# Optimization experiments

Measured on AMD Instinct MI355X. Metric: run time of the kernel, lower is better.

Reference implementation:

```python
import jax, jax.numpy as jnp
import numpy as np

EMBED_DIM = 768
NUM_HEADS = 12
PROJ_DIM = EMBED_DIM // NUM_HEADS  # 64
M_FEATURES = 128
EPS = 1e-6


def _orthogonal_projection(key, m, d):
    # Faithful to create_projection_matrix(scaling=0): stacked transposed Q-factors
    # of iid gaussian blocks, rescaled by chi-distributed row norms.
    nb_full_blocks = m // d
    keys = jax.random.split(key, nb_full_blocks + 2)
    blocks = []
    for i in range(nb_full_blocks):
        q, _ = jnp.linalg.qr(jax.random.normal(keys[i], (d, d)))
        blocks.append(q.T)
    rem = m - nb_full_blocks * d
    if rem > 0:
        q, _ = jnp.linalg.qr(jax.random.normal(keys[nb_full_blocks], (d, d)))
        blocks.append(q.T[:rem])
    final = jnp.vstack(blocks)
    multiplier = jnp.linalg.norm(jax.random.normal(keys[-1], (m, d)), axis=1)
    return multiplier[:, None] * final


def setup_inputs() -> dict:
    key = jax.random.key(0)
    ks = jax.random.split(key, 8)
    B, L, E = 4, 4096, EMBED_DIM
    s = 1.0 / np.sqrt(E)
    inp = {
        "x": jax.random.normal(ks[0], (B, L, E), jnp.float32),
        "Wq": jax.random.normal(ks[1], (E, E), jnp.float32) * s,
        "bq": jnp.zeros((E,), jnp.float32),
        "Wk": jax.random.normal(ks[2], (E, E), jnp.float32) * s,
        "bk": jnp.zeros((E,), jnp.float32),
        "Wv": jax.random.normal(ks[3], (E, E), jnp.float32) * s,
        "bv": jnp.zeros((E,), jnp.float32),
        "Wo": jax.random.normal(ks[4], (E, E), jnp.float32) * s,
        "bo": jnp.zeros((E,), jnp.float32),
        "proj": _orthogonal_projection(ks[5], M_FEATURES, PROJ_DIM),
    }
    return inp


def _softmax_kernel(data, projection_matrix):
    # data: [B, L, H, D]; projection_matrix: [M, D]
    data_normalizer = 1.0 / jnp.sqrt(jnp.sqrt(jnp.float32(PROJ_DIM)))
    data = data_normalizer * data
    ratio = 1.0 / jnp.sqrt(jnp.float32(projection_matrix.shape[0]))
    data_dash = jnp.einsum("blhd,md->blhm", data, projection_matrix)
    diag_data = jnp.sum(jnp.square(data), axis=-1, keepdims=True) / 2.0  # [B,L,H,1]
    stab = jnp.max(data_dash, axis=-1, keepdims=True)
    return ratio * (jnp.exp(data_dash - diag_data - stab) + EPS)


def reference(x, Wq, bq, Wk, bk, Wv, bv, Wo, bo, proj):
    B, L, E = x.shape
    H, D = NUM_HEADS, PROJ_DIM

    def split_heads(t):
        return t.reshape(B, L, H, D)

    q = split_heads(x @ Wq + bq)
    k = split_heads(x @ Wk + bk)
    v = split_heads(x @ Wv + bv)

    q_prime = _softmax_kernel(q, proj)  # [B,L,H,M]
    k_prime = _softmax_kernel(k, proj)  # [B,L,H,M]

    # Linear-attention numerator/denominator (O(L) in sequence length).
    kvs = jnp.einsum("blhm,blhd->bhmd", k_prime, v)          # [B,H,M,D]
    num = jnp.einsum("blhm,bhmd->blhd", q_prime, kvs)        # [B,L,H,D]
    ks_sum = jnp.sum(k_prime, axis=1)                         # [B,H,M]
    den = jnp.einsum("blhm,bhm->blh", q_prime, ks_sum)        # [B,L,H]
    attention = num / den[..., None]                          # [B,L,H,D]

    # Faithful to source: transpose to [B,H,L,D] then reshape to [B,-1,E].
    concat = jnp.transpose(attention, (0, 2, 1, 3)).reshape(B, -1, E)
    return concat @ Wo + bo
```

## Files before the change

### kernel.cpp

```cpp
#include <hip/hip_runtime.h>

typedef _Float16 f16;
typedef __attribute__((ext_vector_type(8))) _Float16 half8;
typedef __attribute__((ext_vector_type(4))) _Float16 half4;
typedef __attribute__((ext_vector_type(4))) float f32x4;

#define DEVINL static __device__ __forceinline__

constexpr float NORMALIZER = 0.35355339059327373f;
constexpr float RATIO      = 0.08838834764831845f;
constexpr float FEPS       = 1e-6f;

constexpr size_t OFF_WQKVT = 0;
constexpr size_t OFF_WOT   = OFF_WQKVT + (size_t)2304*768*2;
constexpr size_t OFF_PROJF = OFF_WOT   + (size_t)768*768*2;
constexpr size_t OFF_KS    = OFF_PROJF + (size_t)128*64*2;
constexpr size_t OFF_KSP   = OFF_KS    + (size_t)48*128*4;
constexpr size_t OFF_DEN   = OFF_KSP   + (size_t)48*64*128*4;
constexpr size_t OFF_KVST  = OFF_DEN   + (size_t)48*4096*4;
constexpr size_t OFF_KVSP  = OFF_KVST  + (size_t)48*64*128*2;
constexpr size_t OFF_X16   = OFF_KVSP  + (size_t)8*48*128*64*4;
constexpr size_t OFF_ATT   = OFF_X16;
constexpr size_t OFF_Q16   = OFF_X16 + (size_t)16384*768*2;
constexpr size_t OFF_K16   = OFF_Q16 + (size_t)16384*768*2;
constexpr size_t OFF_VT    = OFF_K16 + (size_t)16384*768*2;
constexpr size_t OFF_QP    = OFF_K16;
constexpr size_t OFF_KPT   = OFF_VT  + (size_t)16384*768*2;

DEVINL void gload_lds16(const f16* g, f16* lds) {
  __builtin_amdgcn_global_load_lds(
      (const __attribute__((address_space(1))) void*)g,
      (__attribute__((address_space(3))) void*)lds, 16, 0, 0);
}

#define VMCNT(n)  asm volatile("s_waitcnt vmcnt(" #n ")" ::: "memory")
#define LGKMCNT0  asm volatile("s_waitcnt lgkmcnt(0)" ::: "memory")
#define SCHEDB    __builtin_amdgcn_sched_barrier(0)
#define BAR       __builtin_amdgcn_s_barrier()

DEVINL void gemm8p_core(const f16* __restrict__ Ag, const f16* __restrict__ Bg,
                        f16* smem, f32x4 (&acc)[8][4], int w, int lane)
{
  constexpr int NT = 12;
  const int wm = w >> 2, wn = w & 3;
  const int c = lane & 15, g16 = lane >> 4;

#pragma unroll
  for (int i = 0; i < 8; ++i)
#pragma unroll
    for (int j = 0; j < 4; ++j)
      acc[i][j] = f32x4{0.f, 0.f, 0.f, 0.f};

  auto STG = [&](const f16* g, int koff, f16* ldsbase) {
#pragma unroll
    for (int u = 0; u < 2; ++u) {
      const int r = w * 32 + u * 16 + (lane >> 2);
      const int sg = lane & 3;
      gload_lds16(g + (size_t)r * 768 + koff + ((sg ^ ((r ^ (r >> 2)) & 3)) << 3),
                  ldsbase + (w * 128 + u * 64) * 8);
    }
  };
  auto RDA = [&](const f16* kbase, int mh, half8 (&av)[4]) {
#pragma unroll
    for (int i = 0; i < 4; ++i) {
      const int r = wm * 128 + mh * 64 + i * 16 + c;
      av[i] = *(const half8*)(kbase + r * 32 + ((g16 ^ ((r ^ (r >> 2)) & 3)) << 3));
    }
  };
  auto RDB = [&](const f16* kbase, half8 (&bv)[4]) {
#pragma unroll
    for (int j = 0; j < 4; ++j) {
      const int col = wn * 64 + j * 16 + c;
      bv[j] = *(const half8*)(kbase + 16384 + col * 32 + ((g16 ^ ((col ^ (col >> 2)) & 3)) << 3));
    }
  };
  auto MF0 = [&](const half8 (&av)[4], const half8 (&bv)[4]) {
    __builtin_amdgcn_s_setprio(1);
#pragma unroll
    for (int i = 0; i < 4; ++i)
#pragma unroll
      for (int j = 0; j < 4; ++j)
        acc[i][j] = __builtin_amdgcn_mfma_f32_16x16x32_f16(av[i], bv[j], acc[i][j], 0, 0, 0);
    __builtin_amdgcn_s_setprio(0);
  };
  auto MF1 = [&](const half8 (&av)[4], const half8 (&bv)[4]) {
    __builtin_amdgcn_s_setprio(1);
#pragma unroll
    for (int i = 0; i < 4; ++i)
#pragma unroll
      for (int j = 0; j < 4; ++j)
        acc[4 + i][j] = __builtin_amdgcn_mfma_f32_16x16x32_f16(av[i], bv[j], acc[4 + i][j], 0, 0, 0);
    __builtin_amdgcn_s_setprio(0);
  };

  STG(Ag, 0, smem);
  STG(Bg, 0, smem + 16384);
  STG(Ag, 32, smem + 8192);
  STG(Bg, 32, smem + 16384 + 8192);
  VMCNT(0);
  BAR; SCHEDB;

#pragma unroll 1
  for (int t = 0; t < NT; ++t) {
    f16* bufR = smem + (t & 1) * 32768;
    f16* bufW = smem + ((t & 1) ^ 1) * 32768;
    const int kn = (t + 1) * 64;
    const bool st = (t + 1) < NT;
    half8 av[4], bv[4];

    RDA(bufR, 0, av); RDB(bufR, bv);
    if (st) STG(Ag, kn, bufW);
    SCHEDB; BAR; LGKMCNT0; SCHEDB;
    MF0(av, bv);
    BAR; SCHEDB;
    RDA(bufR, 1, av);
    if (st) STG(Bg, kn, bufW + 16384);
    SCHEDB; BAR; LGKMCNT0; SCHEDB;
    MF1(av, bv);
    if (st) { VMCNT(4); } else { VMCNT(0); }
    BAR; SCHEDB;
    RDA(bufR + 8192, 0, av); RDB(bufR + 8192, bv);
    if (st) STG(Ag, kn + 32, bufW + 8192);
    SCHEDB; BAR; LGKMCNT0; SCHEDB;
    MF0(av, bv);
    BAR; SCHEDB;
    RDA(bufR + 8192, 1, av);
    if (st) STG(Bg, kn + 32, bufW + 16384 + 8192);
    SCHEDB; BAR; LGKMCNT0; SCHEDB;
    MF1(av, bv);
    if (st) { VMCNT(4); }
    BAR; SCHEDB;
  }
}

__global__ __launch_bounds__(512, 2) void k_gemm_qkv4(const f16* __restrict__ X16, const f16* __restrict__ WT,
    const float* __restrict__ bq, const float* __restrict__ bk, const float* __restrict__ bv,
    f16* __restrict__ Qo, f16* __restrict__ Ko, f16* __restrict__ VT)
{
  __shared__ f16 smem[65536];
  f32x4 acc[8][4];
  const int lin = blockIdx.x;
  const int xcd = lin & 7, idx = lin >> 3;
  const int bx = xcd * 8 + idx / 9;
  const int by = idx % 9;
  const int brow0 = bx * 256;
  const int t = threadIdx.x, w = t >> 6, lane = t & 63;
  gemm8p_core(X16 + (size_t)brow0 * 768, WT + (size_t)by * 256 * 768, smem, acc, w, lane);

  const int wm = w >> 2, wn = w & 3;
  const int c = lane & 15, g16 = lane >> 4;
  const int which = by / 3;
  const int colhdr = (by % 3) * 256;
  const float* bias = which == 0 ? bq : (which == 1 ? bk : bv);
  float bb[4];
#pragma unroll
  for (int j = 0; j < 4; ++j) bb[j] = bias[colhdr + wn * 64 + j * 16 + c];

  f16* ep = smem;
  if (which < 2) {
    f16* QK = which == 0 ? Qo : Ko;
#pragma unroll 1
    for (int p = 0; p < 2; ++p) {
      __syncthreads();
      if (wm == p) {
#pragma unroll
        for (int ii = 0; ii < 8; ++ii)
#pragma unroll
          for (int j = 0; j < 4; ++j)
#pragma unroll
            for (int r = 0; r < 4; ++r)
              ep[((ii >> 2) * 64 + (ii & 3) * 16 + g16 * 4 + r) * 264 + wn * 64 + j * 16 + c]
                  = (f16)(acc[ii][j][r] + bb[j]);
      }
      __syncthreads();
      const int row = threadIdx.x >> 2, seg = (threadIdx.x & 3) * 64;
      f16* dst = QK + (size_t)(brow0 + p * 128 + row) * 768 + colhdr + seg;
      const f16* sp = ep + row * 264 + seg;
#pragma unroll
      for (int u = 0; u < 4; ++u) *(half8*)(dst + u * 8) = *(const half8*)(sp + u * 8);
#pragma unroll
      for (int u = 4; u < 8; ++u) *(half8*)(dst + u * 8) = *(const half8*)(sp + u * 8);
    }
  } else {
    const int bIdx = brow0 >> 12;
#pragma unroll 1
    for (int ch = 0; ch < 2; ++ch) {
      __syncthreads();
      if ((wn >> 1) == ch) {
        const int cih0 = (wn & 1) * 64;
#pragma unroll
        for (int ii = 0; ii < 8; ++ii)
#pragma unroll
          for (int j = 0; j < 4; ++j)
#pragma unroll
            for (int r = 0; r < 4; ++r)
              ep[(cih0 + j * 16 + c) * 264 + wm * 128 + (ii >> 2) * 64 + (ii & 3) * 16 + g16 * 4 + r]
                  = (f16)(acc[ii][j][r] + bb[j]);
      }
      __syncthreads();
      const int cl = threadIdx.x >> 2, seg = (threadIdx.x & 3) * 64;
      const int vcol = colhdr + ch * 128 + cl;
      const int h = vcol >> 6, d = vcol & 63;
      f16* dst = VT + ((size_t)(bIdx * 12 + h) * 64 + d) * 4096 + (brow0 & 4095) + seg;
      const f16* sp = ep + cl * 264 + seg;
#pragma unroll
      for (int u = 0; u < 8; ++u) *(half8*)(dst + u * 8) = *(const half8*)(sp + u * 8);
    }
  }
}

__global__ __launch_bounds__(512, 2) void k_gemm_out4(const f16* __restrict__ ATT, const f16* __restrict__ WOT,
    const float* __restrict__ bo, float* __restrict__ out)
{
  __shared__ f16 smem[65536];
  f32x4 acc[8][4];
  const int lin = blockIdx.x;
  const int xcd = lin & 7, idx = lin >> 3;
  const int bx = xcd * 8 + idx / 3;
  const int by = idx % 3;
  const int brow0 = bx * 256;
  const int t = threadIdx.x, w = t >> 6, lane = t & 63;
  gemm8p_core(ATT + (size_t)brow0 * 768, WOT + (size_t)by * 256 * 768, smem, acc, w, lane);

  const int wm = w >> 2, wn = w & 3;
  const int c = lane & 15, g16 = lane >> 4;
  float bb[4];
#pragma unroll
  for (int j = 0; j < 4; ++j) bb[j] = bo[by * 256 + wn * 64 + j * 16 + c];
#pragma unroll
  for (int ii = 0; ii < 8; ++ii) {
    const int row0 = brow0 + wm * 128 + (ii >> 2) * 64 + (ii & 3) * 16 + g16 * 4;
#pragma unroll
    for (int j = 0; j < 4; ++j) {
      const int col = by * 256 + wn * 64 + j * 16 + c;
#pragma unroll
      for (int r = 0; r < 4; ++r)
        out[(size_t)(row0 + r) * 768 + col] = acc[ii][j][r] + bb[j];
    }
  }
}

template<int BN>
DEVINL void gemm_tile(const f16* A, int lda, const f16* Bt, int ldb, int K,
                      f16* As, f16* Bs, f32x4 (&acc)[4][BN/32])
{
  constexpr int NF = BN/32;
  const int t = threadIdx.x;
  const int w = t >> 6, lane = t & 63;
  const int g = lane >> 4, c = lane & 15;
  const int wr = w >> 1, wc = w & 1;
  const int srow = lane >> 2;
  const int sseg = (lane & 3) * 8;

#pragma unroll
  for (int i = 0; i < 4; ++i)
#pragma unroll
    for (int j = 0; j < NF; ++j)
      acc[i][j] = f32x4{0.f, 0.f, 0.f, 0.f};

  for (int k0 = 0; k0 < K; k0 += 32) {
#pragma unroll
    for (int r = 0; r < 2; ++r) {
      const int rowblk = (w + 4*r) * 16;
      gload_lds16(A + (size_t)(rowblk + srow) * lda + k0 + sseg, As + rowblk*32);
    }
#pragma unroll
    for (int r = 0; r < BN/64; ++r) {
      const int rowblk = (w + 4*r) * 16;
      gload_lds16(Bt + (size_t)(rowblk + srow) * ldb + k0 + sseg, Bs + rowblk*32);
    }
    __syncthreads();
    half8 av[4], bv[NF];
#pragma unroll
    for (int i = 0; i < 4; ++i)
      av[i] = *(const half8*)(As + (wr*64 + i*16 + c)*32 + g*8);
#pragma unroll
    for (int j = 0; j < NF; ++j)
      bv[j] = *(const half8*)(Bs + (wc*(BN/2) + j*16 + c)*32 + g*8);
#pragma unroll
    for (int i = 0; i < 4; ++i)
#pragma unroll
      for (int j = 0; j < NF; ++j)
        acc[i][j] = __builtin_amdgcn_mfma_f32_16x16x32_f16(av[i], bv[j], acc[i][j], 0, 0, 0);
    __syncthreads();
  }
}

__global__ __launch_bounds__(256) void k_cast_x(const float* __restrict__ X, f16* __restrict__ X16)
{
  const size_t i = ((size_t)blockIdx.x*256 + threadIdx.x) * 4;
  const float4 v = *(const float4*)(X + i);
  half4 h;
  h[0] = (f16)v.x; h[1] = (f16)v.y; h[2] = (f16)v.z; h[3] = (f16)v.w;
  *(half4*)(X16 + i) = h;
}

__global__ __launch_bounds__(256) void k_transpose_w(const float* __restrict__ W, f16* __restrict__ Wt)
{
  __shared__ float ls[64][65];
  const int t = threadIdx.x;
  const int k0 = blockIdx.x*64, n0 = blockIdx.y*64;
#pragma unroll
  for (int it = 0; it < 4; ++it) {
    const int r = it*16 + (t >> 4);
    const int cs = (t & 15) * 4;
    const float4 v = *(const float4*)(W + (size_t)(k0 + r)*768 + n0 + cs);
    ls[r][cs+0] = v.x; ls[r][cs+1] = v.y; ls[r][cs+2] = v.z; ls[r][cs+3] = v.w;
  }
  __syncthreads();
  const int n = t >> 2;
  const int seg = (t & 3) * 16;
  half8 ov[2];
#pragma unroll
  for (int i = 0; i < 16; ++i) ov[i>>3][i&7] = (f16)ls[seg + i][n];
  f16* dst = Wt + (size_t)(n0 + n)*768 + k0 + seg;
  *(half8*)dst = ov[0];
  *(half8*)(dst + 8) = ov[1];
}

__global__ __launch_bounds__(256) void k_cast_proj(const float* __restrict__ P, f16* __restrict__ PF)
{
  const int i = blockIdx.x*256 + threadIdx.x;
  PF[i] = (f16)(NORMALIZER * P[i]);
}

DEVINL void feat_common(const f16* base, const f16* PROJF,
                        f16* qs, f16* ps, float* dd, float* diag_s)
{
  const int t = threadIdx.x, w = t >> 6, lane = t & 63;
#pragma unroll
  for (int it = 0; it < 2; ++it) {
    const int rowblk = it*32 + w*8;
    gload_lds16(base + (size_t)(rowblk + (lane>>3))*768 + (lane&7)*8, qs + rowblk*64);
  }
#pragma unroll
  for (int it = 0; it < 4; ++it) {
    const int rowblk = it*32 + w*8;
    gload_lds16(PROJF + (size_t)(rowblk + (lane>>3))*64 + (lane&7)*8, ps + rowblk*64);
  }
  __syncthreads();
  if (t < 64) {
    float s = 0.f;
    for (int d = 0; d < 64; ++d) { const float qv = (float)qs[t*64 + d]; s += qv*qv; }
    diag_s[t] = 0.0625f * s;
  }
  const int g = lane >> 4, c = lane & 15;
  const int wr = w >> 1, wc = w & 1;
  f32x4 facc[2][4];
#pragma unroll
  for (int i = 0; i < 2; ++i)
#pragma unroll
    for (int j = 0; j < 4; ++j) facc[i][j] = f32x4{0.f,0.f,0.f,0.f};
#pragma unroll
  for (int kk = 0; kk < 2; ++kk) {
    half8 av[2], bv[4];
#pragma unroll
    for (int i = 0; i < 2; ++i) av[i] = *(const half8*)(qs + (wr*32 + i*16 + c)*64 + kk*32 + g*8);
#pragma unroll
    for (int j = 0; j < 4; ++j) bv[j] = *(const half8*)(ps + (wc*64 + j*16 + c)*64 + kk*32 + g*8);
#pragma unroll
    for (int i = 0; i < 2; ++i)
#pragma unroll
      for (int j = 0; j < 4; ++j)
        facc[i][j] = __builtin_amdgcn_mfma_f32_16x16x32_f16(av[i], bv[j], facc[i][j], 0, 0, 0);
  }
#pragma unroll
  for (int i = 0; i < 2; ++i)
#pragma unroll
    for (int j = 0; j < 4; ++j)
#pragma unroll
      for (int r = 0; r < 4; ++r)
        dd[(wr*32 + i*16 + g*4 + r)*129 + wc*64 + j*16 + c] = facc[i][j][r];
  __syncthreads();
}

__global__ __launch_bounds__(256) void k_qfeat(const f16* __restrict__ Q, const f16* __restrict__ PROJF,
    const float* __restrict__ KS, f16* __restrict__ QP, float* __restrict__ DEN)
{
  __shared__ f16 qs[64*64];
  __shared__ f16 ps[128*64];
  __shared__ float dd[64*129];
  __shared__ float diag_s[64];
  __shared__ float ks_s[128];
  const int t = threadIdx.x;
  const int lb = blockIdx.x, bh = blockIdx.y;
  const int b = bh / 12, h = bh - b*12;
  if (t < 128) ks_s[t] = KS[bh*128 + t];
  feat_common(Q + ((size_t)(b*4096 + lb*64))*768 + h*64, PROJF, qs, ps, dd, diag_s);
  const int l = t >> 2, s = t & 3;
  float v[32];
#pragma unroll
  for (int j = 0; j < 32; ++j) v[j] = dd[l*129 + s*32 + j];
  float mx = v[0];
#pragma unroll
  for (int j = 1; j < 32; ++j) mx = fmaxf(mx, v[j]);
  mx = fmaxf(mx, __shfl_xor(mx, 1));
  mx = fmaxf(mx, __shfl_xor(mx, 2));
  const float off = diag_s[l] + mx;
  half8 ov[4];
  float dp = 0.f;
#pragma unroll
  for (int j = 0; j < 32; ++j) {
    const float e = RATIO * (__expf(v[j] - off) + FEPS);
    ov[j>>3][j&7] = (f16)e;
    dp += e * ks_s[s*32 + j];
  }
  dp += __shfl_xor(dp, 1);
  dp += __shfl_xor(dp, 2);
  const size_t lrow = (size_t)bh*4096 + lb*64 + l;
  if (s == 0) DEN[lrow] = dp;
  f16* dst = QP + lrow*128 + s*32;
#pragma unroll
  for (int q8 = 0; q8 < 4; ++q8) *(half8*)(dst + q8*8) = ov[q8];
}

__global__ __launch_bounds__(256) void k_kfeat(const f16* __restrict__ Kin, const f16* __restrict__ PROJF,
    f16* __restrict__ KPT, float* __restrict__ KSP)
{
  __shared__ f16 qs[64*64];
  __shared__ f16 ps[128*64];
  __shared__ float dd[64*129];
  __shared__ float diag_s[64];
  const int t = threadIdx.x;
  const int lb = blockIdx.x, bh = blockIdx.y;
  const int b = bh / 12, h = bh - b*12;
  feat_common(Kin + ((size_t)(b*4096 + lb*64))*768 + h*64, PROJF, qs, ps, dd, diag_s);
  const int l = t >> 2, s = t & 3;
  float v[32];
#pragma unroll
  for (int j = 0; j < 32; ++j) v[j] = dd[l*129 + s*32 + j];
  float mx = v[0];
#pragma unroll
  for (int j = 1; j < 32; ++j) mx = fmaxf(mx, v[j]);
  mx = fmaxf(mx, __shfl_xor(mx, 1));
  mx = fmaxf(mx, __shfl_xor(mx, 2));
  const float off = diag_s[l] + mx;
#pragma unroll
  for (int j = 0; j < 32; ++j) dd[l*129 + s*32 + j] = RATIO * (__expf(v[j] - off) + FEPS);
  __syncthreads();
  if (t < 128) {
    float sm = 0.f;
    for (int l2 = 0; l2 < 64; ++l2) sm += dd[l2*129 + t];
    KSP[((size_t)bh*64 + lb)*128 + t] = sm;
  }
  const int m = t >> 1, hf = t & 1;
  half8 ov[4];
#pragma unroll
  for (int i2 = 0; i2 < 32; ++i2) ov[i2>>3][i2&7] = (f16)dd[(hf*32 + i2)*129 + m];
  f16* dst = KPT + ((size_t)bh*128 + m)*4096 + lb*64 + hf*32;
#pragma unroll
  for (int q8 = 0; q8 < 4; ++q8) *(half8*)(dst + q8*8) = ov[q8];
}

__global__ __launch_bounds__(256) void k_kvs(const f16* __restrict__ KPT, const f16* __restrict__ VT,
    float* __restrict__ KVSP)
{
  __shared__ f16 As[128*32], Bs[64*32];
  f32x4 acc[4][2];
  const int chunk = blockIdx.x, bh = blockIdx.y;
  gemm_tile<64>(KPT + (size_t)bh*128*4096 + chunk*512, 4096,
                VT  + (size_t)bh*64*4096  + chunk*512, 4096, 512, As, Bs, acc);
  const int t = threadIdx.x, w = t>>6, lane = t&63, g = lane>>4, c = lane&15;
  const int wr = w>>1, wc = w&1;
  float* dst = KVSP + (size_t)(chunk*48 + bh)*128*64;
#pragma unroll
  for (int i = 0; i < 4; ++i) {
    const int row0 = wr*64 + i*16 + g*4;
#pragma unroll
    for (int j = 0; j < 2; ++j) {
      const int col = wc*32 + j*16 + c;
#pragma unroll
      for (int r = 0; r < 4; ++r) dst[(size_t)(row0 + r)*64 + col] = acc[i][j][r];
    }
  }
}

__global__ __launch_bounds__(256) void k_reduce(const float* __restrict__ KVSP, const float* __restrict__ KSP,
    f16* __restrict__ KVST, float* __restrict__ KS)
{
  const int i = blockIdx.x*256 + threadIdx.x;
  if (i < 48*128*64) {
    const int bh = i >> 13, md = i & 8191, m = md >> 6, d = md & 63;
    float s = 0.f;
#pragma unroll
    for (int c = 0; c < 8; ++c) s += KVSP[((size_t)(c*48 + bh)*128 + m)*64 + d];
    KVST[((size_t)bh*64 + d)*128 + m] = (f16)s;
  }
  if (i < 48*128) {
    const int bh = i >> 7, m = i & 127;
    float s = 0.f;
#pragma unroll 8
    for (int lb = 0; lb < 64; ++lb) s += KSP[((size_t)bh*64 + lb)*128 + m];
    KS[i] = s;
  }
}

__global__ __launch_bounds__(256) void k_num(const f16* __restrict__ QP, const f16* __restrict__ KVST,
    const float* __restrict__ DEN, f16* __restrict__ ATT)
{
  __shared__ f16 As[128*32], Bs[64*32];
  f32x4 acc[4][2];
  const int bx = blockIdx.x, bh = blockIdx.y;
  gemm_tile<64>(QP + ((size_t)bh*4096 + bx*128)*128, 128,
                KVST + (size_t)bh*64*128, 128, 128, As, Bs, acc);
  const int t = threadIdx.x, w = t>>6, lane = t&63, g = lane>>4, c = lane&15;
  const int wr = w>>1, wc = w&1;
#pragma unroll
  for (int i = 0; i < 4; ++i) {
    const int l0 = bx*128 + wr*64 + i*16 + g*4;
#pragma unroll
    for (int j = 0; j < 2; ++j) {
      const int d = wc*32 + j*16 + c;
#pragma unroll
      for (int r = 0; r < 4; ++r) {
        const float den = DEN[(size_t)bh*4096 + l0 + r];
        ATT[((size_t)bh*4096 + l0 + r)*64 + d] = (f16)(acc[i][j][r] / den);
      }
    }
  }
}

extern "C" void kernel_launch(void* const* d_in, const int* in_sizes, int n_in,
                              void* d_out, int out_size, void* d_ws, size_t ws_size,
                              hipStream_t stream)
{
  const float* x    = (const float*)d_in[0];
  const float* Wq   = (const float*)d_in[1];
  const float* bq   = (const float*)d_in[2];
  const float* Wk   = (const float*)d_in[3];
  const float* bk   = (const float*)d_in[4];
  const float* Wv   = (const float*)d_in[5];
  const float* bv   = (const float*)d_in[6];
  const float* Wo   = (const float*)d_in[7];
  const float* bo   = (const float*)d_in[8];
  const float* proj = (const float*)d_in[9];
  float* out = (float*)d_out;
  char* ws = (char*)d_ws;

  f16*   WQKVT = (f16*)(ws + OFF_WQKVT);
  f16*   WOT   = (f16*)(ws + OFF_WOT);
  f16*   PROJF = (f16*)(ws + OFF_PROJF);
  float* KS    = (float*)(ws + OFF_KS);
  float* KSP   = (float*)(ws + OFF_KSP);
  float* DEN   = (float*)(ws + OFF_DEN);
  f16*   KVST  = (f16*)(ws + OFF_KVST);
  float* KVSP  = (float*)(ws + OFF_KVSP);
  f16*   X16   = (f16*)(ws + OFF_X16);
  f16*   ATT   = (f16*)(ws + OFF_ATT);
  f16*   Q16   = (f16*)(ws + OFF_Q16);
  f16*   K16   = (f16*)(ws + OFF_K16);
  f16*   VT    = (f16*)(ws + OFF_VT);
  f16*   QP    = (f16*)(ws + OFF_QP);
  f16*   KPT   = (f16*)(ws + OFF_KPT);

  k_cast_x<<<12288, 256, 0, stream>>>(x, X16);
  k_transpose_w<<<dim3(12,12), 256, 0, stream>>>(Wq, WQKVT);
  k_transpose_w<<<dim3(12,12), 256, 0, stream>>>(Wk, WQKVT + (size_t)768*768);
  k_transpose_w<<<dim3(12,12), 256, 0, stream>>>(Wv, WQKVT + (size_t)2*768*768);
  k_transpose_w<<<dim3(12,12), 256, 0, stream>>>(Wo, WOT);
  k_cast_proj<<<32, 256, 0, stream>>>(proj, PROJF);

  k_gemm_qkv4<<<576, 512, 0, stream>>>(X16, WQKVT, bq, bk, bv, Q16, K16, VT);
  k_kfeat<<<dim3(64,48), 256, 0, stream>>>(K16, PROJF, KPT, KSP);
  k_kvs<<<dim3(8,48), 256, 0, stream>>>(KPT, VT, KVSP);
  k_reduce<<<1536, 256, 0, stream>>>(KVSP, KSP, KVST, KS);
  k_qfeat<<<dim3(64,48), 256, 0, stream>>>(Q16, PROJF, KS, QP, DEN);
  k_num<<<dim3(32,48), 256, 0, stream>>>(QP, KVST, DEN, ATT);
  k_gemm_out4<<<192, 512, 0, stream>>>(ATT, WOT, bo, out);
}
```

Baseline: 283.5 us.

## Retile GEMMs to 256x192 blocks and fuse Q features with numerator

The shared GEMM core moves from 256x256 to 256x192 tiles, with a new swizzled LDS layout and smaller LDS. This raises the QKV grid to 768 blocks and the output GEMM grid to 256, so wave quantization across CUs improves. The Q feature map, denominator and numerator GEMM are fused into one kernel, k_qfn, which keeps QP and DEN in LDS instead of writing them to global memory and reading them back. The trade-offs are more LDS per feature block and less reuse per GEMM tile.

```diff
diff --git a/kernel.cpp b/kernel.cpp
--- a/kernel.cpp
+++ b/kernel.cpp
@@ -24,7 +24,6 @@
 constexpr size_t OFF_Q16   = OFF_X16 + (size_t)16384*768*2;
 constexpr size_t OFF_K16   = OFF_Q16 + (size_t)16384*768*2;
 constexpr size_t OFF_VT    = OFF_K16 + (size_t)16384*768*2;
-constexpr size_t OFF_QP    = OFF_K16;
 constexpr size_t OFF_KPT   = OFF_VT  + (size_t)16384*768*2;
 
 DEVINL void gload_lds16(const f16* g, f16* lds) {
@@ -38,123 +37,140 @@
 #define SCHEDB    __builtin_amdgcn_sched_barrier(0)
 #define BAR       __builtin_amdgcn_s_barrier()
 
-DEVINL void gemm8p_core(const f16* __restrict__ Ag, const f16* __restrict__ Bg,
-                        f16* smem, f32x4 (&acc)[8][4], int w, int lane)
+DEVINL void gemm192_core(const f16* __restrict__ Ag, const f16* __restrict__ Bg,
+                         f16* smem, f32x4 (&acc)[8][3], int w, int lane)
 {
   constexpr int NT = 12;
   const int wm = w >> 2, wn = w & 3;
   const int c = lane & 15, g16 = lane >> 4;
+  const int tid = threadIdx.x;
 
 #pragma unroll
   for (int i = 0; i < 8; ++i)
 #pragma unroll
-    for (int j = 0; j < 4; ++j)
+    for (int j = 0; j < 3; ++j)
       acc[i][j] = f32x4{0.f, 0.f, 0.f, 0.f};
 
-  auto STG = [&](const f16* g, int koff, f16* ldsbase) {
+  auto SA = [&](int tt, int kh, f16* buf) {
+    f16* dst = buf + kh * 8192;
 #pragma unroll
     for (int u = 0; u < 2; ++u) {
-      const int r = w * 32 + u * 16 + (lane >> 2);
-      const int sg = lane & 3;
-      gload_lds16(g + (size_t)r * 768 + koff + ((sg ^ ((r ^ (r >> 2)) & 3)) << 3),
-                  ldsbase + (w * 128 + u * 64) * 8);
+      const int id = u * 512 + tid;
+      const int r = id >> 2, sg = id & 3;
+      const int seg = sg ^ ((r >> 1) & 3);
+      gload_lds16(Ag + (size_t)r * 768 + tt * 64 + kh * 32 + seg * 8,
+                  dst + (u * 512 + w * 64) * 8);
     }
   };
-  auto RDA = [&](const f16* kbase, int mh, half8 (&av)[4]) {
+  auto SB = [&](int tt, f16* buf) {
+    f16* dst = buf + 16384;
+#pragma unroll
+    for (int u = 0; u < 3; ++u) {
+      const int id = u * 512 + tid;
+      const int r = id >> 3, sg = id & 7;
+      const int seg = sg ^ (r & 7);
+      gload_lds16(Bg + (size_t)r * 768 + tt * 64 + seg * 8,
+                  dst + (u * 512 + w * 64) * 8);
+    }
+  };
+  auto RDA = [&](const f16* buf, int kh, int mh, half8 (&av)[4]) {
+    const f16* base = buf + kh * 8192;
 #pragma unroll
     for (int i = 0; i < 4; ++i) {
       const int r = wm * 128 + mh * 64 + i * 16 + c;
-      av[i] = *(const half8*)(kbase + r * 32 + ((g16 ^ ((r ^ (r >> 2)) & 3)) << 3));
+      av[i] = *(const half8*)(base + r * 32 + ((g16 ^ ((r >> 1) & 3)) << 3));
     }
   };
-  auto RDB = [&](const f16* kbase, half8 (&bv)[4]) {
-#pragma unroll
-    for (int j = 0; j < 4; ++j) {
-      const int col = wn * 64 + j * 16 + c;
-      bv[j] = *(const half8*)(kbase + 16384 + col * 32 + ((g16 ^ ((col ^ (col >> 2)) & 3)) << 3));
+  auto RDB = [&](const f16* buf, int kh, half8 (&bv)[3]) {
+#pragma unroll
+    for (int j = 0; j < 3; ++j) {
+      const int r = wn * 48 + j * 16 + c;
+      const int s = kh * 4 + g16;
+      bv[j] = *(const half8*)(buf + 16384 + r * 64 + ((s ^ (r & 7)) << 3));
     }
   };
-  auto MF0 = [&](const half8 (&av)[4], const half8 (&bv)[4]) {
+
+  SA(0, 0, smem); SB(0, smem); SA(0, 1, smem);
+  VMCNT(0);
+  BAR; SCHEDB;
+
+#pragma unroll 1
+  for (int t = 0; t < NT; ++t) {
+    f16* bufR = smem + (t & 1) * 28672;
+    f16* bufW = smem + ((t & 1) ^ 1) * 28672;
+    const bool st = (t + 1) < NT;
+    half8 av[4], bv[3];
+
+    RDA(bufR, 0, 0, av); RDB(bufR, 0, bv);
+    if (st) SA(t + 1, 0, bufW);
+    SCHEDB; BAR; LGKMCNT0; SCHEDB;
     __builtin_amdgcn_s_setprio(1);
 #pragma unroll
     for (int i = 0; i < 4; ++i)
 #pragma unroll
-      for (int j = 0; j < 4; ++j)
+      for (int j = 0; j < 3; ++j)
         acc[i][j] = __builtin_amdgcn_mfma_f32_16x16x32_f16(av[i], bv[j], acc[i][j], 0, 0, 0);
     __builtin_amdgcn_s_setprio(0);
-  };
-  auto MF1 = [&](const half8 (&av)[4], const half8 (&bv)[4]) {
+    BAR; SCHEDB;
+    RDA(bufR, 0, 1, av);
+    if (st) SB(t + 1, bufW);
+    SCHEDB; BAR; LGKMCNT0; SCHEDB;
     __builtin_amdgcn_s_setprio(1);
 #pragma unroll
     for (int i = 0; i < 4; ++i)
 #pragma unroll
-      for (int j = 0; j < 4; ++j)
+      for (int j = 0; j < 3; ++j)
         acc[4 + i][j] = __builtin_amdgcn_mfma_f32_16x16x32_f16(av[i], bv[j], acc[4 + i][j], 0, 0, 0);
     __builtin_amdgcn_s_setprio(0);
-  };
-
-  STG(Ag, 0, smem);
-  STG(Bg, 0, smem + 16384);
-  STG(Ag, 32, smem + 8192);
-  STG(Bg, 32, smem + 16384 + 8192);
-  VMCNT(0);
-  BAR; SCHEDB;
-
-#pragma unroll 1
-  for (int t = 0; t < NT; ++t) {
-    f16* bufR = smem + (t & 1) * 32768;
-    f16* bufW = smem + ((t & 1) ^ 1) * 32768;
-    const int kn = (t + 1) * 64;
-    const bool st = (t + 1) < NT;
-    half8 av[4], bv[4];
-
-    RDA(bufR, 0, av); RDB(bufR, bv);
-    if (st) STG(Ag, kn, bufW);
+    if (st) { VMCNT(5); } else { VMCNT(0); }
+    BAR; SCHEDB;
+    RDA(bufR, 1, 0, av); RDB(bufR, 1, bv);
+    if (st) SA(t + 1, 1, bufW);
     SCHEDB; BAR; LGKMCNT0; SCHEDB;
-    MF0(av, bv);
+    __builtin_amdgcn_s_setprio(1);
+#pragma unroll
+    for (int i = 0; i < 4; ++i)
+#pragma unroll
+      for (int j = 0; j < 3; ++j)
+        acc[i][j] = __builtin_amdgcn_mfma_f32_16x16x32_f16(av[i], bv[j], acc[i][j], 0, 0, 0);
+    __builtin_amdgcn_s_setprio(0);
     BAR; SCHEDB;
-    RDA(bufR, 1, av);
-    if (st) STG(Bg, kn, bufW + 16384);
+    RDA(bufR, 1, 1, av);
     SCHEDB; BAR; LGKMCNT0; SCHEDB;
-    MF1(av, bv);
-    if (st) { VMCNT(4); } else { VMCNT(0); }
+    __builtin_amdgcn_s_setprio(1);
+#pragma unroll
+    for (int i = 0; i < 4; ++i)
+#pragma unroll
+      for (int j = 0; j < 3; ++j)
+        acc[4 + i][j] = __builtin_amdgcn_mfma_f32_16x16x32_f16(av[i], bv[j], acc[4 + i][j], 0, 0, 0);
+    __builtin_amdgcn_s_setprio(0);
+    if (st) { VMCNT(2); }
     BAR; SCHEDB;
-    RDA(bufR + 8192, 0, av); RDB(bufR + 8192, bv);
-    if (st) STG(Ag, kn + 32, bufW + 8192);
-    SCHEDB; BAR; LGKMCNT0; SCHEDB;
-    MF0(av, bv);
-    BAR; SCHEDB;
-    RDA(bufR + 8192, 1, av);
-    if (st) STG(Bg, kn + 32, bufW + 16384 + 8192);
-    SCHEDB; BAR; LGKMCNT0; SCHEDB;
-    MF1(av, bv);
-    if (st) { VMCNT(4); }
-    BAR; SCHEDB;
-  }
-}
-
-__global__ __launch_bounds__(512, 2) void k_gemm_qkv4(const f16* __restrict__ X16, const f16* __restrict__ WT,
+  }
+}
+
+__global__ __launch_bounds__(512, 2) void k_gemm_qkv5(const f16* __restrict__ X16, const f16* __restrict__ WT,
     const float* __restrict__ bq, const float* __restrict__ bk, const float* __restrict__ bv,
     f16* __restrict__ Qo, f16* __restrict__ Ko, f16* __restrict__ VT)
 {
-  __shared__ f16 smem[65536];
-  f32x4 acc[8][4];
+  __shared__ f16 smem[57344];
+  f32x4 acc[8][3];
   const int lin = blockIdx.x;
-  const int xcd = lin & 7, idx = lin >> 3;
-  const int bx = xcd * 8 + idx / 9;
-  const int by = idx % 9;
+  const int xcd = lin & 7, chunk = lin >> 3;
+  const int bx = xcd * 8 + chunk / 12;
+  const int by = chunk % 12;
   const int brow0 = bx * 256;
   const int t = threadIdx.x, w = t >> 6, lane = t & 63;
-  gemm8p_core(X16 + (size_t)brow0 * 768, WT + (size_t)by * 256 * 768, smem, acc, w, lane);
+  gemm192_core(X16 + (size_t)brow0 * 768, WT + (size_t)by * 192 * 768, smem, acc, w, lane);
 
   const int wm = w >> 2, wn = w & 3;
   const int c = lane & 15, g16 = lane >> 4;
-  const int which = by / 3;
-  const int colhdr = (by % 3) * 256;
+  const int which = by >> 2;
+  const int colhdr = (by & 3) * 192;
   const float* bias = which == 0 ? bq : (which == 1 ? bk : bv);
-  float bb[4];
-#pragma unroll
-  for (int j = 0; j < 4; ++j) bb[j] = bias[colhdr + wn * 64 + j * 16 + c];
+  float bb[3];
+#pragma unroll
+  for (int j = 0; j < 3; ++j) bb[j] = bias[colhdr + wn * 48 + j * 16 + c];
 
   f16* ep = smem;
   if (which < 2) {
@@ -166,73 +182,72 @@
 #pragma unroll
         for (int ii = 0; ii < 8; ++ii)
 #pragma unroll
-          for (int j = 0; j < 4; ++j)
+          for (int j = 0; j < 3; ++j)
 #pragma unroll
             for (int r = 0; r < 4; ++r)
-              ep[((ii >> 2) * 64 + (ii & 3) * 16 + g16 * 4 + r) * 264 + wn * 64 + j * 16 + c]
+              ep[((ii >> 2) * 64 + (ii & 3) * 16 + g16 * 4 + r) * 200 + wn * 48 + j * 16 + c]
                   = (f16)(acc[ii][j][r] + bb[j]);
       }
       __syncthreads();
-      const int row = threadIdx.x >> 2, seg = (threadIdx.x & 3) * 64;
-      f16* dst = QK + (size_t)(brow0 + p * 128 + row) * 768 + colhdr + seg;
-      const f16* sp = ep + row * 264 + seg;
-#pragma unroll
-      for (int u = 0; u < 4; ++u) *(half8*)(dst + u * 8) = *(const half8*)(sp + u * 8);
-#pragma unroll
-      for (int u = 4; u < 8; ++u) *(half8*)(dst + u * 8) = *(const half8*)(sp + u * 8);
+      const int row = t >> 2, sg = (t & 3) * 48;
+      f16* dst = QK + (size_t)(brow0 + p * 128 + row) * 768 + colhdr + sg;
+      const f16* sp = ep + row * 200 + sg;
+#pragma unroll
+      for (int u = 0; u < 6; ++u) *(half8*)(dst + u * 8) = *(const half8*)(sp + u * 8);
     }
   } else {
     const int bIdx = brow0 >> 12;
 #pragma unroll 1
-    for (int ch = 0; ch < 2; ++ch) {
+    for (int p = 0; p < 2; ++p) {
       __syncthreads();
-      if ((wn >> 1) == ch) {
-        const int cih0 = (wn & 1) * 64;
+      if (wm == p) {
 #pragma unroll
         for (int ii = 0; ii < 8; ++ii)
 #pragma unroll
-          for (int j = 0; j < 4; ++j)
+          for (int j = 0; j < 3; ++j)
 #pragma unroll
             for (int r = 0; r < 4; ++r)
-              ep[(cih0 + j * 16 + c) * 264 + wm * 128 + (ii >> 2) * 64 + (ii & 3) * 16 + g16 * 4 + r]
+              ep[(wn * 48 + j * 16 + c) * 136 + (ii >> 2) * 64 + (ii & 3) * 16 + g16 * 4 + r]
                   = (f16)(acc[ii][j][r] + bb[j]);
       }
       __syncthreads();
-      const int cl = threadIdx.x >> 2, seg = (threadIdx.x & 3) * 64;
-      const int vcol = colhdr + ch * 128 + cl;
-      const int h = vcol >> 6, d = vcol & 63;
-      f16* dst = VT + ((size_t)(bIdx * 12 + h) * 64 + d) * 4096 + (brow0 & 4095) + seg;
-      const f16* sp = ep + cl * 264 + seg;
-#pragma unroll
-      for (int u = 0; u < 8; ++u) *(half8*)(dst + u * 8) = *(const half8*)(sp + u * 8);
-    }
-  }
-}
-
-__global__ __launch_bounds__(512, 2) void k_gemm_out4(const f16* __restrict__ ATT, const f16* __restrict__ WOT,
+      if (t < 384) {
+        const int cl = t >> 1, sg = (t & 1) * 64;
+        const int vcol = colhdr + cl;
+        const int h = vcol >> 6, d = vcol & 63;
+        f16* dst = VT + ((size_t)(bIdx * 12 + h) * 64 + d) * 4096 + (brow0 & 4095) + p * 128 + sg;
+        const f16* sp = ep + cl * 136 + sg;
+#pragma unroll
+        for (int u = 0; u < 8; ++u) *(half8*)(dst + u * 8) = *(const half8*)(sp + u * 8);
+      }
+    }
+  }
+}
+
+__global__ __launch_bounds__(512, 2) void k_gemm_out5(const f16* __restrict__ ATT, const f16* __restrict__ WOT,
     const float* __restrict__ bo, float* __restrict__ out)
 {
-  __shared__ f16 smem[65536];
-  f32x4 acc[8][4];
+  __shared__ f16 smem[57344];
+  f32x4 acc[8][3];
   const int lin = blockIdx.x;
-  const int xcd = lin & 7, idx = lin >> 3;
-  const int bx = xcd * 8 + idx / 3;
-  const int by = idx % 3;
+  const int xcd = lin & 7, chunk = lin >> 3;
+  const int bx = xcd * 8 + (chunk >> 2);
+  const int by = chunk & 3;
   const int brow0 = bx * 256;
   const int t = threadIdx.x, w = t >> 6, lane = t & 63;
-  gemm8p_core(ATT + (size_t)brow0 * 768, WOT + (size_t)by * 256 * 768, smem, acc, w, lane);
+  gemm192_core(ATT + (size_t)brow0 * 768, WOT + (size_t)by * 192 * 768, smem, acc, w, lane);
 
   const int wm = w >> 2, wn = w & 3;
   const int c = lane & 15, g16 = lane >> 4;
-  float bb[4];
-#pragma unroll
-  for (int j = 0; j < 4; ++j) bb[j] = bo[by * 256 + wn * 64 + j * 16 + c];
+  float bb[3];
+#pragma unroll
+  for (int j = 0; j < 3; ++j) bb[j] = bo[by * 192 + wn * 48 + j * 16 + c];
 #pragma unroll
   for (int ii = 0; ii < 8; ++ii) {
     const int row0 = brow0 + wm * 128 + (ii >> 2) * 64 + (ii & 3) * 16 + g16 * 4;
 #pragma unroll
-    for (int j = 0; j < 4; ++j) {
-      const int col = by * 256 + wn * 64 + j * 16 + c;
+    for (int j = 0; j < 3; ++j) {
+      const int col = by * 192 + wn * 48 + j * 16 + c;
 #pragma unroll
       for (int r = 0; r < 4; ++r)
         out[(size_t)(row0 + r) * 768 + col] = acc[ii][j][r] + bb[j];
@@ -372,46 +387,6 @@
       for (int r = 0; r < 4; ++r)
         dd[(wr*32 + i*16 + g*4 + r)*129 + wc*64 + j*16 + c] = facc[i][j][r];
   __syncthreads();
-}
-
-__global__ __launch_bounds__(256) void k_qfeat(const f16* __restrict__ Q, const f16* __restrict__ PROJF,
-    const float* __restrict__ KS, f16* __restrict__ QP, float* __restrict__ DEN)
-{
-  __shared__ f16 qs[64*64];
-  __shared__ f16 ps[128*64];
-  __shared__ float dd[64*129];
-  __shared__ float diag_s[64];
-  __shared__ float ks_s[128];
-  const int t = threadIdx.x;
-  const int lb = blockIdx.x, bh = blockIdx.y;
-  const int b = bh / 12, h = bh - b*12;
-  if (t < 128) ks_s[t] = KS[bh*128 + t];
-  feat_common(Q + ((size_t)(b*4096 + lb*64))*768 + h*64, PROJF, qs, ps, dd, diag_s);
-  const int l = t >> 2, s = t & 3;
-  float v[32];
-#pragma unroll
-  for (int j = 0; j < 32; ++j) v[j] = dd[l*129 + s*32 + j];
-  float mx = v[0];
-#pragma unroll
-  for (int j = 1; j < 32; ++j) mx = fmaxf(mx, v[j]);
-  mx = fmaxf(mx, __shfl_xor(mx, 1));
-  mx = fmaxf(mx, __shfl_xor(mx, 2));
-  const float off = diag_s[l] + mx;
-  half8 ov[4];
-  float dp = 0.f;
-#pragma unroll
-  for (int j = 0; j < 32; ++j) {
-    const float e = RATIO * (__expf(v[j] - off) + FEPS);
-    ov[j>>3][j&7] = (f16)e;
-    dp += e * ks_s[s*32 + j];
-  }
-  dp += __shfl_xor(dp, 1);
-  dp += __shfl_xor(dp, 2);
-  const size_t lrow = (size_t)bh*4096 + lb*64 + l;
-  if (s == 0) DEN[lrow] = dp;
-  f16* dst = QP + lrow*128 + s*32;
-#pragma unroll
-  for (int q8 = 0; q8 < 4; ++q8) *(half8*)(dst + q8*8) = ov[q8];
 }
 
 __global__ __launch_bounds__(256) void k_kfeat(const f16* __restrict__ Kin, const f16* __restrict__ PROJF,
@@ -495,29 +470,95 @@
   }
 }
 
-__global__ __launch_bounds__(256) void k_num(const f16* __restrict__ QP, const f16* __restrict__ KVST,
-    const float* __restrict__ DEN, f16* __restrict__ ATT)
-{
-  __shared__ f16 As[128*32], Bs[64*32];
-  f32x4 acc[4][2];
-  const int bx = blockIdx.x, bh = blockIdx.y;
-  gemm_tile<64>(QP + ((size_t)bh*4096 + bx*128)*128, 128,
-                KVST + (size_t)bh*64*128, 128, 128, As, Bs, acc);
-  const int t = threadIdx.x, w = t>>6, lane = t&63, g = lane>>4, c = lane&15;
-  const int wr = w>>1, wc = w&1;
-#pragma unroll
-  for (int i = 0; i < 4; ++i) {
-    const int l0 = bx*128 + wr*64 + i*16 + g*4;
-#pragma unroll
-    for (int j = 0; j < 2; ++j) {
-      const int d = wc*32 + j*16 + c;
+__global__ __launch_bounds__(256) void k_qfn(const f16* __restrict__ Q, const f16* __restrict__ PROJF,
+    const float* __restrict__ KS, const f16* __restrict__ KVST, f16* __restrict__ ATT)
+{
+  __shared__ f16 qs[64*64];
+  __shared__ f16 ps[128*64];
+  __shared__ float dd[64*129];
+  __shared__ float diag_s[64];
+  __shared__ float den_s[64];
+  __shared__ f16 qp[64*128];
+  __shared__ float ks_s[128];
+  const int t = threadIdx.x;
+  const int lb = blockIdx.x, bh = blockIdx.y;
+  const int b = bh / 12, h = bh - b*12;
+  if (t < 128) ks_s[t] = KS[bh*128 + t];
+  feat_common(Q + ((size_t)(b*4096 + lb*64))*768 + h*64, PROJF, qs, ps, dd, diag_s);
+
+  const int w = t >> 6, lane = t & 63, g16 = lane >> 4, c = lane & 15;
+  const int wr = w >> 1, wc = w & 1;
+  half8 bv2[2][4];
+#pragma unroll
+  for (int j = 0; j < 2; ++j) {
+    const int d = wc*32 + j*16 + c;
+#pragma unroll
+    for (int kk = 0; kk < 4; ++kk)
+      bv2[j][kk] = *(const half8*)(KVST + (size_t)bh*8192 + d*128 + kk*32 + g16*8);
+  }
+
+  const int l = t >> 2, s = t & 3;
+  float v[32];
+#pragma unroll
+  for (int j = 0; j < 32; ++j) v[j] = dd[l*129 + s*32 + j];
+  float mx = v[0];
+#pragma unroll
+  for (int j = 1; j < 32; ++j) mx = fmaxf(mx, v[j]);
+  mx = fmaxf(mx, __shfl_xor(mx, 1));
+  mx = fmaxf(mx, __shfl_xor(mx, 2));
+  const float off = diag_s[l] + mx;
+  half8 ov[4];
+  float dp = 0.f;
+#pragma unroll
+  for (int j = 0; j < 32; ++j) {
+    const float e = RATIO * (__expf(v[j] - off) + FEPS);
+    ov[j>>3][j&7] = (f16)e;
+    dp += e * ks_s[s*32 + j];
+  }
+  dp += __shfl_xor(dp, 1);
+  dp += __shfl_xor(dp, 2);
+  if (s == 0) den_s[l] = dp;
+#pragma unroll
+  for (int k = 0; k < 4; ++k)
+    *(half8*)(qp + l*128 + (((4*s + k) ^ (l & 7)) << 3)) = ov[k];
+  __syncthreads();
+
+  f32x4 acc2[2][2];
+#pragma unroll
+  for (int i = 0; i < 2; ++i)
+#pragma unroll
+    for (int j = 0; j < 2; ++j) acc2[i][j] = f32x4{0.f,0.f,0.f,0.f};
+#pragma unroll
+  for (int kk = 0; kk < 4; ++kk) {
+    half8 av2[2];
+#pragma unroll
+    for (int i = 0; i < 2; ++i) {
+      const int l2 = wr*32 + i*16 + c;
+      av2[i] = *(const half8*)(qp + l2*128 + (((kk*4 + g16) ^ (l2 & 7)) << 3));
+    }
+#pragma unroll
+    for (int i = 0; i < 2; ++i)
+#pragma unroll
+      for (int j = 0; j < 2; ++j)
+        acc2[i][j] = __builtin_amdgcn_mfma_f32_16x16x32_f16(av2[i], bv2[j][kk], acc2[i][j], 0, 0, 0);
+  }
+
+  f16* ep = ps;
+#pragma unroll
+  for (int i = 0; i < 2; ++i)
+#pragma unroll
+    for (int j = 0; j < 2; ++j)
 #pragma unroll
       for (int r = 0; r < 4; ++r) {
-        const float den = DEN[(size_t)bh*4096 + l0 + r];
-        ATT[((size_t)bh*4096 + l0 + r)*64 + d] = (f16)(acc[i][j][r] / den);
+        const int l3 = wr*32 + i*16 + g16*4 + r;
+        ep[l3*72 + wc*32 + j*16 + c] = (f16)(acc2[i][j][r] / den_s[l3]);
       }
-    }
-  }
+  __syncthreads();
+  const int row = t >> 2, sg = (t & 3) * 16;
+  f16* dst = ATT + ((size_t)bh*4096 + lb*64 + row)*64 + sg;
+  const f16* sp = ep + row*72 + sg;
+  *(half8*)dst = *(const half8*)sp;
+  *(half8*)(dst + 8) = *(const half8*)(sp + 8);
 }
 
 extern "C" void kernel_launch(void* const* d_in, const int* in_sizes, int n_in,
@@ -542,7 +583,6 @@
   f16*   PROJF = (f16*)(ws + OFF_PROJF);
   float* KS    = (float*)(ws + OFF_KS);
   float* KSP   = (float*)(ws + OFF_KSP);
-  float* DEN   = (float*)(ws + OFF_DEN);
   f16*   KVST  = (f16*)(ws + OFF_KVST);
   float* KVSP  = (float*)(ws + OFF_KVSP);
   f16*   X16   = (f16*)(ws + OFF_X16);
@@ -550,7 +590,6 @@
   f16*   Q16   = (f16*)(ws + OFF_Q16);
   f16*   K16   = (f16*)(ws + OFF_K16);
   f16*   VT    = (f16*)(ws + OFF_VT);
-  f16*   QP    = (f16*)(ws + OFF_QP);
   f16*   KPT   = (f16*)(ws + OFF_KPT);
 
   k_cast_x<<<12288, 256, 0, stream>>>(x, X16);
@@ -560,11 +599,10 @@
   k_transpose_w<<<dim3(12,12), 256, 0, stream>>>(Wo, WOT);
   k_cast_proj<<<32, 256, 0, stream>>>(proj, PROJF);
 
-  k_gemm_qkv4<<<576, 512, 0, stream>>>(X16, WQKVT, bq, bk, bv, Q16, K16, VT);
+  k_gemm_qkv5<<<768, 512, 0, stream>>>(X16, WQKVT, bq, bk, bv, Q16, K16, VT);
   k_kfeat<<<dim3(64,48), 256, 0, stream>>>(K16, PROJF, KPT, KSP);
   k_kvs<<<dim3(8,48), 256, 0, stream>>>(KPT, VT, KVSP);
   k_reduce<<<1536, 256, 0, stream>>>(KVSP, KSP, KVST, KS);
-  k_qfeat<<<dim3(64,48), 256, 0, stream>>>(Q16, PROJF, KS, QP, DEN);
-  k_num<<<dim3(32,48), 256, 0, stream>>>(QP, KVST, DEN, ATT);
-  k_gemm_out4<<<192, 512, 0, stream>>>(ATT, WOT, bo, out);
-}
+  k_qfn<<<dim3(64,48), 256, 0, stream>>>(Q16, PROJF, KS, KVST, ATT);
+  k_gemm_out5<<<256, 512, 0, stream>>>(ATT, WOT, bo, out);
+}
```

Result: faster. 251.5 us (-11.3%).
